# Kernel tuning notes

Hardware: AMD Instinct MI355X
Metric: run time of the kernel (lower is better)

The kernel has to match this reference:

```python
import jax, jax.numpy as jnp
import numpy as np

N = 50000

def _norm_coeffs(edge_index, n):
    # add self-loops, compute symmetric GCN normalization D^-1/2 (A+I) D^-1/2
    loops = jnp.arange(n, dtype=edge_index.dtype)
    src = jnp.concatenate([edge_index[0], loops])
    dst = jnp.concatenate([edge_index[1], loops])
    deg = jax.ops.segment_sum(jnp.ones_like(dst, dtype=jnp.float32), dst, num_segments=n)
    dinv = jnp.where(deg > 0, jax.lax.rsqrt(deg), 0.0)
    norm = dinv[src] * dinv[dst]  # [E+N]
    return src, dst, norm

def _gcn(x, W, b, src, dst, norm, n):
    h = x @ W                                   # [N, out]
    m = h[src] * norm[:, None]                  # [E+N, out] gather + scale
    return jax.ops.segment_sum(m, dst, num_segments=n) + b

def setup_inputs() -> dict:
    key = jax.random.key(0)
    ks = jax.random.split(key, 8)
    d, h = 96, 96
    E = 800000
    return {
        "x": jax.random.normal(ks[0], (N, d), jnp.float32),
        "edge_index": jax.random.randint(ks[1], (2, E), 0, N, dtype=jnp.int64),
        "h_prev": jax.random.normal(ks[2], (N, h), jnp.float32),
        "Wx": jax.random.normal(ks[3], (d, h), jnp.float32) * (1.0 / np.sqrt(d)),
        "bx": jnp.zeros((h,), jnp.float32),
        "Wuh": jax.random.normal(ks[4], (2 * h, h), jnp.float32) * (1.0 / np.sqrt(2 * h)),
        "buh": jnp.zeros((h,), jnp.float32),
        "Wch": jax.random.normal(ks[5], (2 * h, h), jnp.float32) * (1.0 / np.sqrt(2 * h)),
        "bch": jnp.zeros((h,), jnp.float32),
    }

def reference(x, edge_index, h_prev, Wx, bx, Wuh, buh, Wch, bch):
    n = x.shape[0]
    src, dst, norm = _norm_coeffs(edge_index, n)
    x_gcn = _gcn(x, Wx, bx, src, dst, norm, n)
    combined = jnp.concatenate([x_gcn, h_prev], axis=1)
    # original computes gcn_uh(combined) twice for u and r; identical math -> compute once
    g = jax.nn.sigmoid(_gcn(combined, Wuh, buh, src, dst, norm, n))
    u = g
    r = g
    combined_r = jnp.concatenate([x_gcn, r * h_prev], axis=1)
    c = jnp.tanh(_gcn(combined_r, Wch, bch, src, dst, norm, n))
    return u * h_prev + (1.0 - u) * c
```

## Files before the change

### kernel.cpp

```cpp
#include <hip/hip_runtime.h>
#include <hip/hip_bf16.h>

#define D 96
#define CAP 64
typedef long long i64;
typedef unsigned short u16;

typedef __bf16 bf16x8 __attribute__((ext_vector_type(8)));
typedef float f32x4 __attribute__((ext_vector_type(4)));

__device__ __forceinline__ float bf2f(u16 u) {
  union { unsigned u; float f; } x; x.u = ((unsigned)u) << 16; return x.f;
}
__device__ __forceinline__ void unpack8(uint4 p, float* a) {
  a[0] = bf2f((u16)(p.x & 0xffff)); a[1] = bf2f((u16)(p.x >> 16));
  a[2] = bf2f((u16)(p.y & 0xffff)); a[3] = bf2f((u16)(p.y >> 16));
  a[4] = bf2f((u16)(p.z & 0xffff)); a[5] = bf2f((u16)(p.z >> 16));
  a[6] = bf2f((u16)(p.w & 0xffff)); a[7] = bf2f((u16)(p.w >> 16));
}

__device__ __forceinline__ void split8(const float* v8, bf16x8& hi, bf16x8& lo) {
  unsigned hu[4], lu[4];
#pragma unroll
  for (int p = 0; p < 4; p++) {
    float v0 = v8[2 * p], v1 = v8[2 * p + 1];
    unsigned u0 = __float_as_uint(v0), u1 = __float_as_uint(v1);
    hu[p] = (u0 >> 16) | (u1 & 0xffff0000u);
    float l0 = v0 - __uint_as_float(u0 & 0xffff0000u);
    float l1 = v1 - __uint_as_float(u1 & 0xffff0000u);
    lu[p] = (__float_as_uint(l0) >> 16) | (__float_as_uint(l1) & 0xffff0000u);
  }
  union { uint4 q; bf16x8 v; } H, L;
  H.q = make_uint4(hu[0], hu[1], hu[2], hu[3]);
  L.q = make_uint4(lu[0], lu[1], lu[2], lu[3]);
  hi = H.v; lo = L.v;
}

__global__ __launch_bounds__(256) void k_build(
    const int* __restrict__ e32, const i64* __restrict__ e64,
    const unsigned* __restrict__ eiw,
    const float* __restrict__ Wx, const float* __restrict__ Wuh,
    const float* __restrict__ Wch,
    u16* __restrict__ wxh, u16* __restrict__ wxl,
    u16* __restrict__ wuhh, u16* __restrict__ wuhl,
    u16* __restrict__ wchh, u16* __restrict__ wchl,
    uint2* __restrict__ region, int* __restrict__ cntmat,
    int E, int N, int NB) {
  const int tid = threadIdx.x;
  if (blockIdx.x >= 256) {
    int cid = (blockIdx.x - 256) * 256 + tid;
    const float* W; u16 *oh, *ol; int loc;
    if (cid < 1152) { W = Wx; oh = wxh; ol = wxl; loc = cid; }
    else if (cid < 3456) { W = Wuh; oh = wuhh; ol = wuhl; loc = cid - 1152; }
    else if (cid < 5760) { W = Wch; oh = wchh; ol = wchl; loc = cid - 3456; }
    else return;
    int oct = loc / 96;
    int j = loc - oct * 96;
    int k0 = oct * 8;
    unsigned hu[4], lu[4];
#pragma unroll
    for (int p = 0; p < 4; p++) {
      float v0 = W[(size_t)(k0 + 2 * p) * D + j];
      float v1 = W[(size_t)(k0 + 2 * p + 1) * D + j];
      unsigned u0 = __float_as_uint(v0), u1 = __float_as_uint(v1);
      hu[p] = (u0 >> 16) | (u1 & 0xffff0000u);
      float l0 = v0 - __uint_as_float(u0 & 0xffff0000u);
      float l1 = v1 - __uint_as_float(u1 & 0xffff0000u);
      lu[p] = (__float_as_uint(l0) >> 16) | (__float_as_uint(l1) & 0xffff0000u);
    }
    *(uint4*)&oh[(size_t)loc * 8] = make_uint4(hu[0], hu[1], hu[2], hu[3]);
    *(uint4*)&ol[(size_t)loc * 8] = make_uint4(lu[0], lu[1], lu[2], lu[3]);
    return;
  }
  __shared__ unsigned fsh[256];
  __shared__ int lofs[256];
  {
    unsigned a = 0;
    int lim = (E < 2048) ? E : 2048;
    for (int j = tid; j < lim; j += 256) a |= eiw[2 * j + 1];
    fsh[tid] = a;
    __syncthreads();
    if (tid < 128) fsh[tid] |= fsh[tid + 128];
    __syncthreads();
    if (tid < 64) {
      unsigned b = fsh[tid] | fsh[tid + 64];
#pragma unroll
      for (int off = 32; off > 0; off >>= 1) b |= __shfl_down(b, off, 64);
      if (tid == 0) fsh[0] = b;
    }
    __syncthreads();
  }
  const int f = (fsh[0] == 0) ? 1 : 0;
  lofs[tid] = 0;
  __syncthreads();
  const int blk = blockIdx.x;
  const int chunk = (E + 255) / 256;
  const int lo = blk * chunk;
  const int hi = min(E, lo + chunk);
  for (int i = lo + tid; i < hi; i += 256) {
    int d, s;
    if (f) { d = (int)e64[(size_t)E + i]; s = (int)e64[i]; }
    else   { d = e32[(size_t)E + i];      s = e32[i]; }
    if ((unsigned)d >= (unsigned)N || (unsigned)s >= (unsigned)N) continue;
    int q = d >> 8;
    int r = atomicAdd(&lofs[q], 1);
    if (r < CAP)
      region[((size_t)q * 256 + blk) * CAP + r] = make_uint2((unsigned)s, (unsigned)d);
  }
  __syncthreads();
  if (tid < NB) cntmat[blk * 256 + tid] = min(lofs[tid], CAP);
}

__global__ __launch_bounds__(256) void k_csr(const uint2* __restrict__ region,
                                             const int* __restrict__ cntmat,
                                             int* __restrict__ deg,
                                             int* __restrict__ csrp, int NB) {
  __shared__ int ldeg[256];
  __shared__ int lcsr[256 * CAP];
  const int tid = threadIdx.x;
  const int b = blockIdx.x;
  ldeg[tid] = 0;
  __syncthreads();
  int cnt = cntmat[tid * 256 + b];
  const uint2* cell = region + ((size_t)b * 256 + tid) * CAP;
  for (int k = 0; k < cnt; k++) {
    uint2 e = cell[k];
    int node = (int)(e.y & 255u);
    int r = atomicAdd(&ldeg[node], 1);
    if (r < CAP) lcsr[node * CAP + r] = (int)e.x;
  }
  __syncthreads();
  deg[(b << 8) + tid] = ldeg[tid];
  const uint4* src = (const uint4*)lcsr;
  uint4* dst = (uint4*)(csrp + ((size_t)b << 8) * CAP);
#pragma unroll
  for (int it = 0; it < (256 * CAP) / 4 / 256; it++)
    dst[tid + it * 256] = src[tid + it * 256];
}

template <int KTOT, int MODE>
__global__ __launch_bounds__(128) void gemm_mfma(
    const float* __restrict__ xin, const float* __restrict__ xg,
    const float* __restrict__ hprev, const float* __restrict__ gmul,
    const u16* __restrict__ whi, const u16* __restrict__ wlo,
    const int* __restrict__ deg, __hip_bfloat16* __restrict__ t, int N) {
  constexpr bool KS = (KTOT == 192);
  __shared__ float lcomb[64][25];
  const int l = threadIdx.x & 63;
  const int wv = threadIdx.x >> 6;
  const int j16 = l & 15;
  const int koct = l >> 4;
  const int rb = KS ? blockIdx.x * 16 : blockIdx.x * 32 + wv * 16;
  const int row = rb + j16;
  const bool rok = row < N;

  f32x4 c0, c1, c2, c3, c4, c5;
#pragma unroll
  for (int i = 0; i < 4; i++) { c0[i] = 0.f; c1[i] = 0.f; c2[i] = 0.f;
                                c3[i] = 0.f; c4[i] = 0.f; c5[i] = 0.f; }

#define COLT(CT, ACC) do {                                                  \
    union { uint4 q; bf16x8 v; } Bh, Bl;                                    \
    const size_t wb = (so + (CT)*16 + j16) * 8;                             \
    Bh.q = *(const uint4*)&whi[wb];                                         \
    Bl.q = *(const uint4*)&wlo[wb];                                         \
    ACC = __builtin_amdgcn_mfma_f32_16x16x32_bf16(ah, Bh.v, ACC, 0, 0, 0);  \
    ACC = __builtin_amdgcn_mfma_f32_16x16x32_bf16(al, Bh.v, ACC, 0, 0, 0);  \
    ACC = __builtin_amdgcn_mfma_f32_16x16x32_bf16(ah, Bl.v, ACC, 0, 0, 0);  \
  } while (0)

#pragma unroll
  for (int ss = 0; ss < 3; ss++) {
    const int s = KS ? (wv * 3 + ss) : ss;
    float a8[8] = {0.f, 0.f, 0.f, 0.f, 0.f, 0.f, 0.f, 0.f};
    if (rok) {
      const int kb = ss * 32 + koct * 8;
      const float* src;
      if (MODE == 0) src = xin;
      else if (!KS || wv == 0) src = xg;
      else src = hprev;
      float4 va = *(const float4*)&src[(size_t)row * D + kb];
      float4 vb = *(const float4*)&src[(size_t)row * D + kb + 4];
      if (MODE == 2 && KS && wv == 1) {
        float4 ga = *(const float4*)&gmul[(size_t)row * D + kb];
        float4 gb = *(const float4*)&gmul[(size_t)row * D + kb + 4];
        va.x *= ga.x; va.y *= ga.y; va.z *= ga.z; va.w *= ga.w;
        vb.x *= gb.x; vb.y *= gb.y; vb.z *= gb.z; vb.w *= gb.w;
      }
      a8[0] = va.x; a8[1] = va.y; a8[2] = va.z; a8[3] = va.w;
      a8[4] = vb.x; a8[5] = vb.y; a8[6] = vb.z; a8[7] = vb.w;
    }
    bf16x8 ah, al;
    split8(a8, ah, al);
    const size_t so = (size_t)(s * 4 + koct) * 96;
    COLT(0, c0); COLT(1, c1); COLT(2, c2);
    COLT(3, c3); COLT(4, c4); COLT(5, c5);
  }
#undef COLT

  if (KS) {
    if (wv == 1) {
#pragma unroll
      for (int r = 0; r < 4; r++) {
        lcomb[l][0 + r]  = c0[r]; lcomb[l][4 + r]  = c1[r];
        lcomb[l][8 + r]  = c2[r]; lcomb[l][12 + r] = c3[r];
        lcomb[l][16 + r] = c4[r]; lcomb[l][20 + r] = c5[r];
      }
    }
    __syncthreads();
    if (wv == 1) return;
#pragma unroll
    for (int r = 0; r < 4; r++) {
      c0[r] += lcomb[l][0 + r];  c1[r] += lcomb[l][4 + r];
      c2[r] += lcomb[l][8 + r];  c3[r] += lcomb[l][12 + r];
      c4[r] += lcomb[l][16 + r]; c5[r] += lcomb[l][20 + r];
    }
  }

  const int r0 = rb + koct * 4;
  float dv[4];
#pragma unroll
  for (int r = 0; r < 4; r++)
    dv[r] = (r0 + r < N) ? rsqrtf((float)deg[r0 + r] + 1.0f) : 0.f;
#pragma unroll
  for (int r = 0; r < 4; r++) {
    int orow = r0 + r;
    if (orow >= N) continue;
    __hip_bfloat16* tp = &t[(size_t)orow * D + j16];
    tp[0]  = __float2bfloat16(c0[r] * dv[r]);
    tp[16] = __float2bfloat16(c1[r] * dv[r]);
    tp[32] = __float2bfloat16(c2[r] * dv[r]);
    tp[48] = __float2bfloat16(c3[r] * dv[r]);
    tp[64] = __float2bfloat16(c4[r] * dv[r]);
    tp[80] = __float2bfloat16(c5[r] * dv[r]);
  }
}

template <int MODE>
__global__ __launch_bounds__(192) void gather_fin(
    const __hip_bfloat16* __restrict__ t, const int* __restrict__ deg,
    const int* __restrict__ csrp,
    const float* __restrict__ bias,
    const float* __restrict__ g, const float* __restrict__ hprev,
    float* __restrict__ outf, int N, int n1, int n2) {
  __shared__ int lidx[16 * 65];
  __shared__ int lsort[16 * 65];
  __shared__ int lcnt[16][4];
  __shared__ int lbase[16][4];
  __shared__ int lpl[16][4];
  __shared__ int ldeg[16];
  const int tid = threadIdx.x;
  const int vbase = blockIdx.x * 16;
#pragma unroll
  for (int it = 0; it < 6; it++) {
    int i = tid + it * 192;
    if (i < 1024) {
      int n = i >> 6, j = i & 63;
      lidx[n * 65 + j] = csrp[((size_t)(vbase + n)) * CAP + j];
    }
  }
  if (tid < 16) ldeg[tid] = deg[vbase + tid];
  if (tid >= 96 && tid < 160) {
    int n = (tid - 96) >> 2, s = (tid - 96) & 3;
    lcnt[n][s] = 0; lpl[n][s] = 0;
  }
  __syncthreads();
  const int n = tid / 12;
  const int c8 = tid - n * 12;
  const int v = vbase + n;
  const int nb = min(ldeg[n], CAP);
  for (int j = c8; j < nb; j += 12) {
    int s = lidx[n * 65 + j];
    int sg = (s >= n1) + (s >= n2);
    atomicAdd(&lcnt[n][sg], 1);
  }
  __syncthreads();
  if (tid < 16) {
    lbase[tid][0] = 0;
    lbase[tid][1] = lcnt[tid][0];
    lbase[tid][2] = lcnt[tid][0] + lcnt[tid][1];
  }
  __syncthreads();
  for (int j = c8; j < nb; j += 12) {
    int s = lidx[n * 65 + j];
    int sg = (s >= n1) + (s >= n2);
    int r = atomicAdd(&lpl[n][sg], 1);
    lsort[n * 65 + lbase[n][sg] + r] = s;
  }
  __syncthreads();

  const uint4* t8 = (const uint4*)t;
  float acc[8] = {0.f, 0.f, 0.f, 0.f, 0.f, 0.f, 0.f, 0.f};
  if (v < N) unpack8(t8[(size_t)v * 12 + c8], acc);
  const int* ip = &lsort[n * 65];
  int j = 0;
  for (; j + 8 <= nb; j += 8) {
    int s0 = ip[j],     s1 = ip[j + 1], s2 = ip[j + 2], s3 = ip[j + 3];
    int s4 = ip[j + 4], s5 = ip[j + 5], s6 = ip[j + 6], s7 = ip[j + 7];
    uint4 p0 = t8[(size_t)s0 * 12 + c8];
    uint4 p1 = t8[(size_t)s1 * 12 + c8];
    uint4 p2 = t8[(size_t)s2 * 12 + c8];
    uint4 p3 = t8[(size_t)s3 * 12 + c8];
    uint4 p4 = t8[(size_t)s4 * 12 + c8];
    uint4 p5 = t8[(size_t)s5 * 12 + c8];
    uint4 p6 = t8[(size_t)s6 * 12 + c8];
    uint4 p7 = t8[(size_t)s7 * 12 + c8];
    float a0[8], a1[8], a2[8], a3[8], a4[8], a5[8], a6[8], a7[8];
    unpack8(p0, a0); unpack8(p1, a1); unpack8(p2, a2); unpack8(p3, a3);
    unpack8(p4, a4); unpack8(p5, a5); unpack8(p6, a6); unpack8(p7, a7);
#pragma unroll
    for (int q = 0; q < 8; q++)
      acc[q] += ((a0[q] + a1[q]) + (a2[q] + a3[q])) + ((a4[q] + a5[q]) + (a6[q] + a7[q]));
  }
  for (; j + 4 <= nb; j += 4) {
    int s0 = ip[j], s1 = ip[j + 1], s2 = ip[j + 2], s3 = ip[j + 3];
    uint4 p0 = t8[(size_t)s0 * 12 + c8];
    uint4 p1 = t8[(size_t)s1 * 12 + c8];
    uint4 p2 = t8[(size_t)s2 * 12 + c8];
    uint4 p3 = t8[(size_t)s3 * 12 + c8];
    float a0[8], a1[8], a2[8], a3[8];
    unpack8(p0, a0); unpack8(p1, a1); unpack8(p2, a2); unpack8(p3, a3);
#pragma unroll
    for (int q = 0; q < 8; q++) acc[q] += (a0[q] + a1[q]) + (a2[q] + a3[q]);
  }
  for (; j < nb; j++) {
    int s = ip[j];
    float a0[8];
    unpack8(t8[(size_t)s * 12 + c8], a0);
#pragma unroll
    for (int q = 0; q < 8; q++) acc[q] += a0[q];
  }
  if (v >= N) return;
  float dv = rsqrtf((float)ldeg[n] + 1.0f);
  float4 bA = ((const float4*)bias)[c8 * 2];
  float4 bB = ((const float4*)bias)[c8 * 2 + 1];
  float z[8] = {dv * acc[0] + bA.x, dv * acc[1] + bA.y, dv * acc[2] + bA.z, dv * acc[3] + bA.w,
                dv * acc[4] + bB.x, dv * acc[5] + bB.y, dv * acc[6] + bB.z, dv * acc[7] + bB.w};
  const size_t oidx = (size_t)v * 12 + c8;
  float4 oA, oB;
  if (MODE == 1) {
    oA = make_float4(z[0], z[1], z[2], z[3]);
    oB = make_float4(z[4], z[5], z[6], z[7]);
  } else if (MODE == 2) {
    oA = make_float4(1.0f / (1.0f + expf(-z[0])), 1.0f / (1.0f + expf(-z[1])),
                     1.0f / (1.0f + expf(-z[2])), 1.0f / (1.0f + expf(-z[3])));
    oB = make_float4(1.0f / (1.0f + expf(-z[4])), 1.0f / (1.0f + expf(-z[5])),
                     1.0f / (1.0f + expf(-z[6])), 1.0f / (1.0f + expf(-z[7])));
  } else {
    float4 uA = ((const float4*)g)[oidx * 2], uB = ((const float4*)g)[oidx * 2 + 1];
    float4 hA = ((const float4*)hprev)[oidx * 2], hB = ((const float4*)hprev)[oidx * 2 + 1];
    oA = make_float4(uA.x * hA.x + (1.0f - uA.x) * tanhf(z[0]),
                     uA.y * hA.y + (1.0f - uA.y) * tanhf(z[1]),
                     uA.z * hA.z + (1.0f - uA.z) * tanhf(z[2]),
                     uA.w * hA.w + (1.0f - uA.w) * tanhf(z[3]));
    oB = make_float4(uB.x * hB.x + (1.0f - uB.x) * tanhf(z[4]),
                     uB.y * hB.y + (1.0f - uB.y) * tanhf(z[5]),
                     uB.z * hB.z + (1.0f - uB.z) * tanhf(z[6]),
                     uB.w * hB.w + (1.0f - uB.w) * tanhf(z[7]));
  }
  ((float4*)outf)[oidx * 2] = oA;
  ((float4*)outf)[oidx * 2 + 1] = oB;
}

extern "C" void kernel_launch(void* const* d_in, const int* in_sizes, int n_in,
                              void* d_out, int out_size, void* d_ws, size_t ws_size,
                              hipStream_t stream) {
  const float* x = (const float*)d_in[0];
  const int* ei32 = (const int*)d_in[1];
  const i64* ei64 = (const i64*)d_in[1];
  const unsigned* eiw = (const unsigned*)d_in[1];
  const float* hp = (const float*)d_in[2];
  const float* Wx = (const float*)d_in[3];
  const float* bx = (const float*)d_in[4];
  const float* Wuh = (const float*)d_in[5];
  const float* buh = (const float*)d_in[6];
  const float* Wch = (const float*)d_in[7];
  const float* bch = (const float*)d_in[8];
  float* out = (float*)d_out;

  const int N = in_sizes[0] / D;
  const int E = in_sizes[1] / 2;
  const size_t NF = (size_t)N * D;
  const int NB = (N + 255) >> 8;
  const int R = NB << 8;
  const int n1 = N / 3, n2 = 2 * (N / 3);

  char* base = (char*)d_ws;
  u16* wxh = (u16*)(base + 256);
  u16* wxl = wxh + 9216;
  u16* wuhh = wxl + 9216;
  u16* wuhl = wuhh + 18432;
  u16* wchh = wuhl + 18432;
  u16* wchl = wchh + 18432;
  int* deg = (int*)(wchl + 18432);
  int* cntmat = deg + R;
  uint2* region = (uint2*)(cntmat + 65536);
  int* csrp = (int*)(region + (size_t)NB * 256 * CAP);
  __hip_bfloat16* t = (__hip_bfloat16*)(csrp + (size_t)R * CAP);
  float* xg = (float*)((char*)t + NF * 2);
  float* g = xg + NF;

  const int gb16 = (N + 15) / 16;
  const int gb32 = (N + 31) / 32;
  const int fb = (N + 15) / 16;

  k_build<<<279, 256, 0, stream>>>(ei32, ei64, eiw, Wx, Wuh, Wch,
                                   wxh, wxl, wuhh, wuhl, wchh, wchl,
                                   region, cntmat, E, N, NB);
  k_csr<<<NB, 256, 0, stream>>>(region, cntmat, deg, csrp, NB);

  gemm_mfma<96, 0><<<gb32, 128, 0, stream>>>(x, nullptr, nullptr, nullptr, wxh, wxl, deg, t, N);
  gather_fin<1><<<fb, 192, 0, stream>>>(t, deg, csrp, bx, nullptr, nullptr, xg, N, n1, n2);

  gemm_mfma<192, 1><<<gb16, 128, 0, stream>>>(nullptr, xg, hp, nullptr, wuhh, wuhl, deg, t, N);
  gather_fin<2><<<fb, 192, 0, stream>>>(t, deg, csrp, buh, nullptr, nullptr, g, N, n1, n2);

  gemm_mfma<192, 2><<<gb16, 128, 0, stream>>>(nullptr, xg, hp, g, wchh, wchl, deg, t, N);
  gather_fin<3><<<fb, 192, 0, stream>>>(t, deg, csrp, bch, g, hp, out, N, n1, n2);
}
```

Before: 264.7 us.

## Fuse GEMMs into CSR build and neighbor-gather kernels, ping-pong transformed buffers

The first x@Wx GEMM moves into the CSR-building kernel and reuses the degree counts already held in shared memory. Each aggregation kernel now also runs the next layer's MFMA GEMM on its 16 finished rows, taking activations from shared memory. Two bf16 buffers alternate so that reads and writes never alias, which cuts eight launches to five. The source-range sorting of neighbor indices, meant for cache locality, is dropped. In exchange the k_csr block does serial GEMM work with a large LDS footprint, and a third of the threads in the fused kernels sit idle during the GEMM.

```diff
diff --git a/kernel.cpp b/kernel.cpp
--- a/kernel.cpp
+++ b/kernel.cpp
@@ -111,10 +111,12 @@
   if (tid < NB) cntmat[blk * 256 + tid] = min(lofs[tid], CAP);
 }
 
-__global__ __launch_bounds__(256) void k_csr(const uint2* __restrict__ region,
-                                             const int* __restrict__ cntmat,
-                                             int* __restrict__ deg,
-                                             int* __restrict__ csrp, int NB) {
+__global__ __launch_bounds__(256) void k_csr_g1(
+    const uint2* __restrict__ region, const int* __restrict__ cntmat,
+    int* __restrict__ deg, int* __restrict__ csrp,
+    const float* __restrict__ x,
+    const u16* __restrict__ whi, const u16* __restrict__ wlo,
+    __hip_bfloat16* __restrict__ t, int NB, int N) {
   __shared__ int ldeg[256];
   __shared__ int lcsr[256 * CAP];
   const int tid = threadIdx.x;
@@ -136,30 +138,12 @@
 #pragma unroll
   for (int it = 0; it < (256 * CAP) / 4 / 256; it++)
     dst[tid + it * 256] = src[tid + it * 256];
-}
-
-template <int KTOT, int MODE>
-__global__ __launch_bounds__(128) void gemm_mfma(
-    const float* __restrict__ xin, const float* __restrict__ xg,
-    const float* __restrict__ hprev, const float* __restrict__ gmul,
-    const u16* __restrict__ whi, const u16* __restrict__ wlo,
-    const int* __restrict__ deg, __hip_bfloat16* __restrict__ t, int N) {
-  constexpr bool KS = (KTOT == 192);
-  __shared__ float lcomb[64][25];
-  const int l = threadIdx.x & 63;
-  const int wv = threadIdx.x >> 6;
+
+  const int l = tid & 63;
+  const int wv = tid >> 6;
   const int j16 = l & 15;
   const int koct = l >> 4;
-  const int rb = KS ? blockIdx.x * 16 : blockIdx.x * 32 + wv * 16;
-  const int row = rb + j16;
-  const bool rok = row < N;
-
-  f32x4 c0, c1, c2, c3, c4, c5;
-#pragma unroll
-  for (int i = 0; i < 4; i++) { c0[i] = 0.f; c1[i] = 0.f; c2[i] = 0.f;
-                                c3[i] = 0.f; c4[i] = 0.f; c5[i] = 0.f; }
-
-#define COLT(CT, ACC) do {                                                  \
+#define COLT1(CT, ACC) do {                                                 \
     union { uint4 q; bf16x8 v; } Bh, Bl;                                    \
     const size_t wb = (so + (CT)*16 + j16) * 8;                             \
     Bh.q = *(const uint4*)&whi[wb];                                         \
@@ -168,131 +152,81 @@
     ACC = __builtin_amdgcn_mfma_f32_16x16x32_bf16(al, Bh.v, ACC, 0, 0, 0);  \
     ACC = __builtin_amdgcn_mfma_f32_16x16x32_bf16(ah, Bl.v, ACC, 0, 0, 0);  \
   } while (0)
-
-#pragma unroll
-  for (int ss = 0; ss < 3; ss++) {
-    const int s = KS ? (wv * 3 + ss) : ss;
-    float a8[8] = {0.f, 0.f, 0.f, 0.f, 0.f, 0.f, 0.f, 0.f};
-    if (rok) {
+#pragma unroll 1
+  for (int tt = 0; tt < 4; tt++) {
+    const int rloc = wv * 64 + tt * 16;
+    const int row = (b << 8) + rloc + j16;
+    const bool rok = row < N;
+    f32x4 c0, c1, c2, c3, c4, c5;
+#pragma unroll
+    for (int i = 0; i < 4; i++) { c0[i] = 0.f; c1[i] = 0.f; c2[i] = 0.f;
+                                  c3[i] = 0.f; c4[i] = 0.f; c5[i] = 0.f; }
+#pragma unroll
+    for (int ss = 0; ss < 3; ss++) {
       const int kb = ss * 32 + koct * 8;
-      const float* src;
-      if (MODE == 0) src = xin;
-      else if (!KS || wv == 0) src = xg;
-      else src = hprev;
-      float4 va = *(const float4*)&src[(size_t)row * D + kb];
-      float4 vb = *(const float4*)&src[(size_t)row * D + kb + 4];
-      if (MODE == 2 && KS && wv == 1) {
-        float4 ga = *(const float4*)&gmul[(size_t)row * D + kb];
-        float4 gb = *(const float4*)&gmul[(size_t)row * D + kb + 4];
-        va.x *= ga.x; va.y *= ga.y; va.z *= ga.z; va.w *= ga.w;
-        vb.x *= gb.x; vb.y *= gb.y; vb.z *= gb.z; vb.w *= gb.w;
+      float a8[8] = {0.f, 0.f, 0.f, 0.f, 0.f, 0.f, 0.f, 0.f};
+      if (rok) {
+        float4 va = *(const float4*)&x[(size_t)row * D + kb];
+        float4 vb = *(const float4*)&x[(size_t)row * D + kb + 4];
+        a8[0] = va.x; a8[1] = va.y; a8[2] = va.z; a8[3] = va.w;
+        a8[4] = vb.x; a8[5] = vb.y; a8[6] = vb.z; a8[7] = vb.w;
       }
-      a8[0] = va.x; a8[1] = va.y; a8[2] = va.z; a8[3] = va.w;
-      a8[4] = vb.x; a8[5] = vb.y; a8[6] = vb.z; a8[7] = vb.w;
-    }
-    bf16x8 ah, al;
-    split8(a8, ah, al);
-    const size_t so = (size_t)(s * 4 + koct) * 96;
-    COLT(0, c0); COLT(1, c1); COLT(2, c2);
-    COLT(3, c3); COLT(4, c4); COLT(5, c5);
-  }
-#undef COLT
-
-  if (KS) {
-    if (wv == 1) {
-#pragma unroll
-      for (int r = 0; r < 4; r++) {
-        lcomb[l][0 + r]  = c0[r]; lcomb[l][4 + r]  = c1[r];
-        lcomb[l][8 + r]  = c2[r]; lcomb[l][12 + r] = c3[r];
-        lcomb[l][16 + r] = c4[r]; lcomb[l][20 + r] = c5[r];
-      }
-    }
-    __syncthreads();
-    if (wv == 1) return;
+      bf16x8 ah, al;
+      split8(a8, ah, al);
+      const size_t so = (size_t)(ss * 4 + koct) * 96;
+      COLT1(0, c0); COLT1(1, c1); COLT1(2, c2);
+      COLT1(3, c3); COLT1(4, c4); COLT1(5, c5);
+    }
+    const int r0loc = rloc + koct * 4;
 #pragma unroll
     for (int r = 0; r < 4; r++) {
-      c0[r] += lcomb[l][0 + r];  c1[r] += lcomb[l][4 + r];
-      c2[r] += lcomb[l][8 + r];  c3[r] += lcomb[l][12 + r];
-      c4[r] += lcomb[l][16 + r]; c5[r] += lcomb[l][20 + r];
-    }
-  }
-
-  const int r0 = rb + koct * 4;
-  float dv[4];
-#pragma unroll
-  for (int r = 0; r < 4; r++)
-    dv[r] = (r0 + r < N) ? rsqrtf((float)deg[r0 + r] + 1.0f) : 0.f;
-#pragma unroll
-  for (int r = 0; r < 4; r++) {
-    int orow = r0 + r;
-    if (orow >= N) continue;
-    __hip_bfloat16* tp = &t[(size_t)orow * D + j16];
-    tp[0]  = __float2bfloat16(c0[r] * dv[r]);
-    tp[16] = __float2bfloat16(c1[r] * dv[r]);
-    tp[32] = __float2bfloat16(c2[r] * dv[r]);
-    tp[48] = __float2bfloat16(c3[r] * dv[r]);
-    tp[64] = __float2bfloat16(c4[r] * dv[r]);
-    tp[80] = __float2bfloat16(c5[r] * dv[r]);
-  }
-}
-
-template <int MODE>
-__global__ __launch_bounds__(192) void gather_fin(
-    const __hip_bfloat16* __restrict__ t, const int* __restrict__ deg,
-    const int* __restrict__ csrp,
-    const float* __restrict__ bias,
-    const float* __restrict__ g, const float* __restrict__ hprev,
-    float* __restrict__ outf, int N, int n1, int n2) {
+      int lr0 = r0loc + r;
+      int orow = (b << 8) + lr0;
+      if (orow >= N) continue;
+      float dvv = rsqrtf((float)ldeg[lr0] + 1.0f);
+      __hip_bfloat16* tp = &t[(size_t)orow * D + j16];
+      tp[0]  = __float2bfloat16(c0[r] * dvv);
+      tp[16] = __float2bfloat16(c1[r] * dvv);
+      tp[32] = __float2bfloat16(c2[r] * dvv);
+      tp[48] = __float2bfloat16(c3[r] * dvv);
+      tp[64] = __float2bfloat16(c4[r] * dvv);
+      tp[80] = __float2bfloat16(c5[r] * dvv);
+    }
+  }
+#undef COLT1
+}
+
+template <int PHASE>
+__global__ __launch_bounds__(192) void k_fuse(
+    const __hip_bfloat16* __restrict__ tin, const int* __restrict__ deg,
+    const int* __restrict__ csrp, const float* __restrict__ bias,
+    const float* __restrict__ xgin, const float* __restrict__ hprev,
+    const u16* __restrict__ whi, const u16* __restrict__ wlo,
+    float* __restrict__ vout, __hip_bfloat16* __restrict__ tout, int N) {
   __shared__ int lidx[16 * 65];
-  __shared__ int lsort[16 * 65];
-  __shared__ int lcnt[16][4];
-  __shared__ int lbase[16][4];
-  __shared__ int lpl[16][4];
   __shared__ int ldeg[16];
+  __shared__ float vl[16][100];
+  __shared__ float lcomb[64][25];
   const int tid = threadIdx.x;
   const int vbase = blockIdx.x * 16;
 #pragma unroll
   for (int it = 0; it < 6; it++) {
     int i = tid + it * 192;
     if (i < 1024) {
-      int n = i >> 6, j = i & 63;
-      lidx[n * 65 + j] = csrp[((size_t)(vbase + n)) * CAP + j];
+      int n2 = i >> 6, j2 = i & 63;
+      lidx[n2 * 65 + j2] = csrp[((size_t)(vbase + n2)) * CAP + j2];
     }
   }
   if (tid < 16) ldeg[tid] = deg[vbase + tid];
-  if (tid >= 96 && tid < 160) {
-    int n = (tid - 96) >> 2, s = (tid - 96) & 3;
-    lcnt[n][s] = 0; lpl[n][s] = 0;
-  }
   __syncthreads();
   const int n = tid / 12;
   const int c8 = tid - n * 12;
   const int v = vbase + n;
   const int nb = min(ldeg[n], CAP);
-  for (int j = c8; j < nb; j += 12) {
-    int s = lidx[n * 65 + j];
-    int sg = (s >= n1) + (s >= n2);
-    atomicAdd(&lcnt[n][sg], 1);
-  }
-  __syncthreads();
-  if (tid < 16) {
-    lbase[tid][0] = 0;
-    lbase[tid][1] = lcnt[tid][0];
-    lbase[tid][2] = lcnt[tid][0] + lcnt[tid][1];
-  }
-  __syncthreads();
-  for (int j = c8; j < nb; j += 12) {
-    int s = lidx[n * 65 + j];
-    int sg = (s >= n1) + (s >= n2);
-    int r = atomicAdd(&lpl[n][sg], 1);
-    lsort[n * 65 + lbase[n][sg] + r] = s;
-  }
-  __syncthreads();
-
-  const uint4* t8 = (const uint4*)t;
+  const uint4* t8 = (const uint4*)tin;
   float acc[8] = {0.f, 0.f, 0.f, 0.f, 0.f, 0.f, 0.f, 0.f};
   if (v < N) unpack8(t8[(size_t)v * 12 + c8], acc);
-  const int* ip = &lsort[n * 65];
+  const int* ip = &lidx[n * 65];
   int j = 0;
   for (; j + 8 <= nb; j += 8) {
     int s0 = ip[j],     s1 = ip[j + 1], s2 = ip[j + 2], s3 = ip[j + 3];
@@ -330,34 +264,194 @@
 #pragma unroll
     for (int q = 0; q < 8; q++) acc[q] += a0[q];
   }
+  {
+    float dvv = rsqrtf((float)ldeg[n] + 1.0f);
+    float4 bA = ((const float4*)bias)[c8 * 2];
+    float4 bB = ((const float4*)bias)[c8 * 2 + 1];
+    float z[8] = {dvv * acc[0] + bA.x, dvv * acc[1] + bA.y,
+                  dvv * acc[2] + bA.z, dvv * acc[3] + bA.w,
+                  dvv * acc[4] + bB.x, dvv * acc[5] + bB.y,
+                  dvv * acc[6] + bB.z, dvv * acc[7] + bB.w};
+    if (PHASE == 2) {
+#pragma unroll
+      for (int q = 0; q < 8; q++) z[q] = 1.0f / (1.0f + expf(-z[q]));
+    }
+#pragma unroll
+    for (int q = 0; q < 8; q++) vl[n][c8 * 8 + q] = (v < N) ? z[q] : 0.f;
+    if (v < N) {
+      const size_t oidx = (size_t)v * 12 + c8;
+      ((float4*)vout)[oidx * 2]     = make_float4(z[0], z[1], z[2], z[3]);
+      ((float4*)vout)[oidx * 2 + 1] = make_float4(z[4], z[5], z[6], z[7]);
+    }
+  }
+  __syncthreads();
+  const int l = tid & 63;
+  const int wv = tid >> 6;
+  const int j16 = l & 15;
+  const int koct = l >> 4;
+  const bool act = tid < 128;
+  f32x4 c0, c1, c2, c3, c4, c5;
+#pragma unroll
+  for (int i = 0; i < 4; i++) { c0[i] = 0.f; c1[i] = 0.f; c2[i] = 0.f;
+                                c3[i] = 0.f; c4[i] = 0.f; c5[i] = 0.f; }
+#define COLT2(CT, ACC) do {                                                 \
+    union { uint4 q; bf16x8 v; } Bh, Bl;                                    \
+    const size_t wb = (so + (CT)*16 + j16) * 8;                             \
+    Bh.q = *(const uint4*)&whi[wb];                                         \
+    Bl.q = *(const uint4*)&wlo[wb];                                         \
+    ACC = __builtin_amdgcn_mfma_f32_16x16x32_bf16(ah, Bh.v, ACC, 0, 0, 0);  \
+    ACC = __builtin_amdgcn_mfma_f32_16x16x32_bf16(al, Bh.v, ACC, 0, 0, 0);  \
+    ACC = __builtin_amdgcn_mfma_f32_16x16x32_bf16(ah, Bl.v, ACC, 0, 0, 0);  \
+  } while (0)
+  if (act) {
+    const int row = vbase + j16;
+    const bool rok = row < N;
+#pragma unroll
+    for (int ss = 0; ss < 3; ss++) {
+      const int kb = ss * 32 + koct * 8;
+      float a8[8] = {0.f, 0.f, 0.f, 0.f, 0.f, 0.f, 0.f, 0.f};
+      if (wv == 0) {
+        if (PHASE == 1) {
+#pragma unroll
+          for (int q = 0; q < 8; q++) a8[q] = vl[j16][kb + q];
+        } else if (rok) {
+          float4 va = *(const float4*)&xgin[(size_t)row * D + kb];
+          float4 vb = *(const float4*)&xgin[(size_t)row * D + kb + 4];
+          a8[0] = va.x; a8[1] = va.y; a8[2] = va.z; a8[3] = va.w;
+          a8[4] = vb.x; a8[5] = vb.y; a8[6] = vb.z; a8[7] = vb.w;
+        }
+      } else if (rok) {
+        float4 va = *(const float4*)&hprev[(size_t)row * D + kb];
+        float4 vb = *(const float4*)&hprev[(size_t)row * D + kb + 4];
+        a8[0] = va.x; a8[1] = va.y; a8[2] = va.z; a8[3] = va.w;
+        a8[4] = vb.x; a8[5] = vb.y; a8[6] = vb.z; a8[7] = vb.w;
+        if (PHASE == 2) {
+#pragma unroll
+          for (int q = 0; q < 8; q++) a8[q] *= vl[j16][kb + q];
+        }
+      }
+      bf16x8 ah, al;
+      split8(a8, ah, al);
+      const size_t so = (size_t)((wv * 3 + ss) * 4 + koct) * 96;
+      COLT2(0, c0); COLT2(1, c1); COLT2(2, c2);
+      COLT2(3, c3); COLT2(4, c4); COLT2(5, c5);
+    }
+  }
+#undef COLT2
+  if (act && wv == 1) {
+#pragma unroll
+    for (int r = 0; r < 4; r++) {
+      lcomb[l][0 + r]  = c0[r]; lcomb[l][4 + r]  = c1[r];
+      lcomb[l][8 + r]  = c2[r]; lcomb[l][12 + r] = c3[r];
+      lcomb[l][16 + r] = c4[r]; lcomb[l][20 + r] = c5[r];
+    }
+  }
+  __syncthreads();
+  if (!(act && wv == 0)) return;
+#pragma unroll
+  for (int r = 0; r < 4; r++) {
+    c0[r] += lcomb[l][0 + r];  c1[r] += lcomb[l][4 + r];
+    c2[r] += lcomb[l][8 + r];  c3[r] += lcomb[l][12 + r];
+    c4[r] += lcomb[l][16 + r]; c5[r] += lcomb[l][20 + r];
+  }
+  const int r0 = koct * 4;
+#pragma unroll
+  for (int r = 0; r < 4; r++) {
+    int orow = vbase + r0 + r;
+    if (orow >= N) continue;
+    float dvv = rsqrtf((float)ldeg[r0 + r] + 1.0f);
+    __hip_bfloat16* tp = &tout[(size_t)orow * D + j16];
+    tp[0]  = __float2bfloat16(c0[r] * dvv);
+    tp[16] = __float2bfloat16(c1[r] * dvv);
+    tp[32] = __float2bfloat16(c2[r] * dvv);
+    tp[48] = __float2bfloat16(c3[r] * dvv);
+    tp[64] = __float2bfloat16(c4[r] * dvv);
+    tp[80] = __float2bfloat16(c5[r] * dvv);
+  }
+}
+
+__global__ __launch_bounds__(192) void k_gfin(
+    const __hip_bfloat16* __restrict__ tin, const int* __restrict__ deg,
+    const int* __restrict__ csrp, const float* __restrict__ bias,
+    const float* __restrict__ g, const float* __restrict__ hprev,
+    float* __restrict__ outf, int N) {
+  __shared__ int lidx[16 * 65];
+  __shared__ int ldeg[16];
+  const int tid = threadIdx.x;
+  const int vbase = blockIdx.x * 16;
+#pragma unroll
+  for (int it = 0; it < 6; it++) {
+    int i = tid + it * 192;
+    if (i < 1024) {
+      int n2 = i >> 6, j2 = i & 63;
+      lidx[n2 * 65 + j2] = csrp[((size_t)(vbase + n2)) * CAP + j2];
+    }
+  }
+  if (tid < 16) ldeg[tid] = deg[vbase + tid];
+  __syncthreads();
+  const int n = tid / 12;
+  const int c8 = tid - n * 12;
+  const int v = vbase + n;
   if (v >= N) return;
-  float dv = rsqrtf((float)ldeg[n] + 1.0f);
+  const uint4* t8 = (const uint4*)tin;
+  float acc[8];
+  unpack8(t8[(size_t)v * 12 + c8], acc);
+  const int nb = min(ldeg[n], CAP);
+  const int* ip = &lidx[n * 65];
+  int j = 0;
+  for (; j + 8 <= nb; j += 8) {
+    int s0 = ip[j],     s1 = ip[j + 1], s2 = ip[j + 2], s3 = ip[j + 3];
+    int s4 = ip[j + 4], s5 = ip[j + 5], s6 = ip[j + 6], s7 = ip[j + 7];
+    uint4 p0 = t8[(size_t)s0 * 12 + c8];
+    uint4 p1 = t8[(size_t)s1 * 12 + c8];
+    uint4 p2 = t8[(size_t)s2 * 12 + c8];
+    uint4 p3 = t8[(size_t)s3 * 12 + c8];
+    uint4 p4 = t8[(size_t)s4 * 12 + c8];
+    uint4 p5 = t8[(size_t)s5 * 12 + c8];
+    uint4 p6 = t8[(size_t)s6 * 12 + c8];
+    uint4 p7 = t8[(size_t)s7 * 12 + c8];
+    float a0[8], a1[8], a2[8], a3[8], a4[8], a5[8], a6[8], a7[8];
+    unpack8(p0, a0); unpack8(p1, a1); unpack8(p2, a2); unpack8(p3, a3);
+    unpack8(p4, a4); unpack8(p5, a5); unpack8(p6, a6); unpack8(p7, a7);
+#pragma unroll
+    for (int q = 0; q < 8; q++)
+      acc[q] += ((a0[q] + a1[q]) + (a2[q] + a3[q])) + ((a4[q] + a5[q]) + (a6[q] + a7[q]));
+  }
+  for (; j + 4 <= nb; j += 4) {
+    int s0 = ip[j], s1 = ip[j + 1], s2 = ip[j + 2], s3 = ip[j + 3];
+    uint4 p0 = t8[(size_t)s0 * 12 + c8];
+    uint4 p1 = t8[(size_t)s1 * 12 + c8];
+    uint4 p2 = t8[(size_t)s2 * 12 + c8];
+    uint4 p3 = t8[(size_t)s3 * 12 + c8];
+    float a0[8], a1[8], a2[8], a3[8];
+    unpack8(p0, a0); unpack8(p1, a1); unpack8(p2, a2); unpack8(p3, a3);
+#pragma unroll
+    for (int q = 0; q < 8; q++) acc[q] += (a0[q] + a1[q]) + (a2[q] + a3[q]);
+  }
+  for (; j < nb; j++) {
+    int s = ip[j];
+    float a0[8];
+    unpack8(t8[(size_t)s * 12 + c8], a0);
+#pragma unroll
+    for (int q = 0; q < 8; q++) acc[q] += a0[q];
+  }
+  float dvv = rsqrtf((float)ldeg[n] + 1.0f);
   float4 bA = ((const float4*)bias)[c8 * 2];
   float4 bB = ((const float4*)bias)[c8 * 2 + 1];
-  float z[8] = {dv * acc[0] + bA.x, dv * acc[1] + bA.y, dv * acc[2] + bA.z, dv * acc[3] + bA.w,
-                dv * acc[4] + bB.x, dv * acc[5] + bB.y, dv * acc[6] + bB.z, dv * acc[7] + bB.w};
+  float z[8] = {dvv * acc[0] + bA.x, dvv * acc[1] + bA.y, dvv * acc[2] + bA.z,
+                dvv * acc[3] + bA.w, dvv * acc[4] + bB.x, dvv * acc[5] + bB.y,
+                dvv * acc[6] + bB.z, dvv * acc[7] + bB.w};
   const size_t oidx = (size_t)v * 12 + c8;
-  float4 oA, oB;
-  if (MODE == 1) {
-    oA = make_float4(z[0], z[1], z[2], z[3]);
-    oB = make_float4(z[4], z[5], z[6], z[7]);
-  } else if (MODE == 2) {
-    oA = make_float4(1.0f / (1.0f + expf(-z[0])), 1.0f / (1.0f + expf(-z[1])),
-                     1.0f / (1.0f + expf(-z[2])), 1.0f / (1.0f + expf(-z[3])));
-    oB = make_float4(1.0f / (1.0f + expf(-z[4])), 1.0f / (1.0f + expf(-z[5])),
-                     1.0f / (1.0f + expf(-z[6])), 1.0f / (1.0f + expf(-z[7])));
-  } else {
-    float4 uA = ((const float4*)g)[oidx * 2], uB = ((const float4*)g)[oidx * 2 + 1];
-    float4 hA = ((const float4*)hprev)[oidx * 2], hB = ((const float4*)hprev)[oidx * 2 + 1];
-    oA = make_float4(uA.x * hA.x + (1.0f - uA.x) * tanhf(z[0]),
-                     uA.y * hA.y + (1.0f - uA.y) * tanhf(z[1]),
-                     uA.z * hA.z + (1.0f - uA.z) * tanhf(z[2]),
-                     uA.w * hA.w + (1.0f - uA.w) * tanhf(z[3]));
-    oB = make_float4(uB.x * hB.x + (1.0f - uB.x) * tanhf(z[4]),
-                     uB.y * hB.y + (1.0f - uB.y) * tanhf(z[5]),
-                     uB.z * hB.z + (1.0f - uB.z) * tanhf(z[6]),
-                     uB.w * hB.w + (1.0f - uB.w) * tanhf(z[7]));
-  }
+  float4 uA = ((const float4*)g)[oidx * 2], uB = ((const float4*)g)[oidx * 2 + 1];
+  float4 hA = ((const float4*)hprev)[oidx * 2], hB = ((const float4*)hprev)[oidx * 2 + 1];
+  float4 oA = make_float4(uA.x * hA.x + (1.0f - uA.x) * tanhf(z[0]),
+                          uA.y * hA.y + (1.0f - uA.y) * tanhf(z[1]),
+                          uA.z * hA.z + (1.0f - uA.z) * tanhf(z[2]),
+                          uA.w * hA.w + (1.0f - uA.w) * tanhf(z[3]));
+  float4 oB = make_float4(uB.x * hB.x + (1.0f - uB.x) * tanhf(z[4]),
+                          uB.y * hB.y + (1.0f - uB.y) * tanhf(z[5]),
+                          uB.z * hB.z + (1.0f - uB.z) * tanhf(z[6]),
+                          uB.w * hB.w + (1.0f - uB.w) * tanhf(z[7]));
   ((float4*)outf)[oidx * 2] = oA;
   ((float4*)outf)[oidx * 2 + 1] = oB;
 }
@@ -383,7 +477,6 @@
   const size_t NF = (size_t)N * D;
   const int NB = (N + 255) >> 8;
   const int R = NB << 8;
-  const int n1 = N / 3, n2 = 2 * (N / 3);
 
   char* base = (char*)d_ws;
   u16* wxh = (u16*)(base + 256);
@@ -396,25 +489,20 @@
   int* cntmat = deg + R;
   uint2* region = (uint2*)(cntmat + 65536);
   int* csrp = (int*)(region + (size_t)NB * 256 * CAP);
-  __hip_bfloat16* t = (__hip_bfloat16*)(csrp + (size_t)R * CAP);
-  float* xg = (float*)((char*)t + NF * 2);
+  __hip_bfloat16* tA = (__hip_bfloat16*)(csrp + (size_t)R * CAP);
+  __hip_bfloat16* tB = tA + NF;
+  float* xg = (float*)(tB + NF);
   float* g = xg + NF;
 
-  const int gb16 = (N + 15) / 16;
-  const int gb32 = (N + 31) / 32;
   const int fb = (N + 15) / 16;
 
   k_build<<<279, 256, 0, stream>>>(ei32, ei64, eiw, Wx, Wuh, Wch,
                                    wxh, wxl, wuhh, wuhl, wchh, wchl,
                                    region, cntmat, E, N, NB);
-  k_csr<<<NB, 256, 0, stream>>>(region, cntmat, deg, csrp, NB);
-
-  gemm_mfma<96, 0><<<gb32, 128, 0, stream>>>(x, nullptr, nullptr, nullptr, wxh, wxl, deg, t, N);
-  gather_fin<1><<<fb, 192, 0, stream>>>(t, deg, csrp, bx, nullptr, nullptr, xg, N, n1, n2);
-
-  gemm_mfma<192, 1><<<gb16, 128, 0, stream>>>(nullptr, xg, hp, nullptr, wuhh, wuhl, deg, t, N);
-  gather_fin<2><<<fb, 192, 0, stream>>>(t, deg, csrp, buh, nullptr, nullptr, g, N, n1, n2);
-
-  gemm_mfma<192, 2><<<gb16, 128, 0, stream>>>(nullptr, xg, hp, g, wchh, wchl, deg, t, N);
-  gather_fin<3><<<fb, 192, 0, stream>>>(t, deg, csrp, bch, g, hp, out, N, n1, n2);
-}
+  k_csr_g1<<<NB, 256, 0, stream>>>(region, cntmat, deg, csrp, x, wxh, wxl, tA, NB, N);
+  k_fuse<1><<<fb, 192, 0, stream>>>(tA, deg, csrp, bx, nullptr, hp,
+                                    wuhh, wuhl, xg, tB, N);
+  k_fuse<2><<<fb, 192, 0, stream>>>(tB, deg, csrp, buh, xg, hp,
+                                    wchh, wchl, g, tA, N);
+  k_gfin<<<fb, 192, 0, stream>>>(tA, deg, csrp, bch, g, hp, out, N);
+}
```

Result: no change. 263.3 us (-0.5%).
